# Kernel optimization log

Measured on AMD Instinct MI355X. Metric: run time of the kernel, lower is better.

## Reference

```python
import jax, jax.numpy as jnp
import numpy as np

_CODEBOOK = np.array([
 [-1,-1,-1,-1,-1,-1,-1,-1,-1,-1],[-1,-1,-1,-1,1,1,-1,-1,-1,1],[-1,-1,-1,1,-1,-1,-1,-1,1,1],[-1,-1,-1,1,1,1,-1,-1,1,-1],
 [-1,-1,1,-1,-1,-1,-1,1,1,-1],[-1,-1,1,-1,1,1,-1,1,1,1],[-1,-1,1,1,-1,-1,-1,1,-1,1],[-1,-1,1,1,1,1,-1,1,-1,-1],
 [-1,1,-1,-1,-1,-1,1,1,-1,-1],[-1,1,-1,-1,1,1,1,1,-1,1],[-1,1,-1,1,-1,-1,1,1,1,1],[-1,1,-1,1,1,1,1,1,1,-1],
 [-1,1,1,-1,-1,-1,1,-1,1,-1],[-1,1,1,-1,1,1,1,-1,1,1],[-1,1,1,1,-1,-1,1,-1,-1,1],[-1,1,1,1,1,1,1,-1,-1,-1],
 [1,-1,-1,-1,-1,1,1,-1,-1,-1],[1,-1,-1,-1,1,-1,1,-1,-1,1],[1,-1,-1,1,-1,1,1,-1,1,1],[1,-1,-1,1,1,-1,1,-1,1,-1],
 [1,-1,1,-1,-1,1,1,1,1,-1],[1,-1,1,-1,1,-1,1,1,1,1],[1,-1,1,1,-1,1,1,1,-1,1],[1,-1,1,1,1,-1,1,1,-1,-1],
 [1,1,-1,-1,-1,1,-1,1,-1,-1],[1,1,-1,-1,1,-1,-1,1,-1,1],[1,1,-1,1,-1,1,-1,1,1,1],[1,1,-1,1,1,-1,-1,1,1,-1],
 [1,1,1,-1,-1,1,-1,-1,1,-1],[1,1,1,-1,1,-1,-1,-1,1,1],[1,1,1,1,-1,1,-1,-1,-1,1],[1,1,1,1,1,-1,-1,-1,-1,-1]],
 dtype=np.float32)

def setup_inputs() -> dict:
    key = jax.random.key(0)
    B, N, D = 64, 65536, 10
    signal = jax.random.normal(key, (B, N, D), dtype=jnp.float32)
    codebook = jnp.asarray(_CODEBOOK)  # [32, 10]
    return {"signal": signal, "codebook": codebook}

def reference(signal, codebook):
    # Euclidean distances to all 32 codewords via Gram trick: [B, N, 32]
    x2 = jnp.sum(signal * signal, axis=-1, keepdims=True)          # [B, N, 1]
    c2 = jnp.sum(codebook * codebook, axis=-1)                      # [32]
    xc = jnp.einsum('bnd,kd->bnk', signal, codebook)                # [B, N, 32]
    d2 = jnp.maximum(x2 + c2 - 2.0 * xc, 0.0)
    distances = jnp.sqrt(d2)
    soft_assignments = jax.nn.softmax(-distances, axis=2)           # [B, N, 32]
    most_like = jnp.argmax(soft_assignments, axis=2)                # [B, N]
    softdecision = codebook[most_like]                              # [B, N, 10]
    return softdecision
```

## Files before the change

### kernel.cpp

```cpp
#include <hip/hip_runtime.h>
#include <stdint.h>

#define PTS    256
#define DIM    10
#define STRIDE 11
#define NVEC   ((PTS * DIM) / 4)

__device__ constexpr float CB[32][10] = {
 {-1,-1,-1,-1,-1,-1,-1,-1,-1,-1},{-1,-1,-1,-1,1,1,-1,-1,-1,1},{-1,-1,-1,1,-1,-1,-1,-1,1,1},{-1,-1,-1,1,1,1,-1,-1,1,-1},
 {-1,-1,1,-1,-1,-1,-1,1,1,-1},{-1,-1,1,-1,1,1,-1,1,1,1},{-1,-1,1,1,-1,-1,-1,1,-1,1},{-1,-1,1,1,1,1,-1,1,-1,-1},
 {-1,1,-1,-1,-1,-1,1,1,-1,-1},{-1,1,-1,-1,1,1,1,1,-1,1},{-1,1,-1,1,-1,-1,1,1,1,1},{-1,1,-1,1,1,1,1,1,1,-1},
 {-1,1,1,-1,-1,-1,1,-1,1,-1},{-1,1,1,-1,1,1,1,-1,1,1},{-1,1,1,1,-1,-1,1,-1,-1,1},{-1,1,1,1,1,1,1,-1,-1,-1},
 {1,-1,-1,-1,-1,1,1,-1,-1,-1},{1,-1,-1,-1,1,-1,1,-1,-1,1},{1,-1,-1,1,-1,1,1,-1,1,1},{1,-1,-1,1,1,-1,1,-1,1,-1},
 {1,-1,1,-1,-1,1,1,1,1,-1},{1,-1,1,-1,1,-1,1,1,1,1},{1,-1,1,1,-1,1,1,1,-1,1},{1,-1,1,1,1,-1,1,1,-1,-1},
 {1,1,-1,-1,-1,1,-1,1,-1,-1},{1,1,-1,-1,1,-1,-1,1,-1,1},{1,1,-1,1,-1,1,-1,1,1,1},{1,1,-1,1,1,-1,-1,1,1,-1},
 {1,1,1,-1,-1,1,-1,-1,1,-1},{1,1,1,-1,1,-1,-1,-1,1,1},{1,1,1,1,-1,1,-1,-1,-1,1},{1,1,1,1,1,-1,-1,-1,-1,-1}};

__global__ __launch_bounds__(PTS) void softdec_kernel(
    const float* __restrict__ sig, float* __restrict__ out)
{
    __shared__ float sIn [PTS * STRIDE];
    __shared__ float sOut[PTS * STRIDE];
    const int tid = threadIdx.x;
    const size_t base = (size_t)blockIdx.x * (PTS * DIM);

    const float4* __restrict__ gin = (const float4*)(sig + base);
    #pragma unroll
    for (int it = 0; it < 3; ++it) {
        const int i = tid + it * PTS;
        if (i < NVEC) {
            const float4 v = gin[i];
            const float vv[4] = {v.x, v.y, v.z, v.w};
            #pragma unroll
            for (int j = 0; j < 4; ++j) {
                const int gg = i * 4 + j;
                const int p  = gg / DIM;
                const int c  = gg - p * DIM;
                sIn[p * STRIDE + c] = vv[j];
            }
        }
    }
    __syncthreads();

    float x[DIM];
    #pragma unroll
    for (int j = 0; j < DIM; ++j) x[j] = sIn[tid * STRIDE + j];

    float best = -1e30f;
    int   bi   = 0;
    #pragma unroll
    for (int k = 0; k < 32; ++k) {
        float s = 0.0f;
        #pragma unroll
        for (int j = 0; j < DIM; ++j)
            s = (CB[k][j] > 0.0f) ? (s + x[j]) : (s - x[j]);
        if (s > best) { best = s; bi = k; }
    }

    #pragma unroll
    for (int j = 0; j < DIM; ++j)
        sOut[tid * STRIDE + j] = CB[bi][j];
    __syncthreads();

    float4* __restrict__ gout = (float4*)(out + base);
    #pragma unroll
    for (int it = 0; it < 3; ++it) {
        const int i = tid + it * PTS;
        if (i < NVEC) {
            float4 v;
            float* vv = (float*)&v;
            #pragma unroll
            for (int j = 0; j < 4; ++j) {
                const int gg = i * 4 + j;
                const int p  = gg / DIM;
                const int c  = gg - p * DIM;
                vv[j] = sOut[p * STRIDE + c];
            }
            gout[i] = v;
        }
    }
}

extern "C" void kernel_launch(void* const* d_in, const int* in_sizes, int n_in,
                              void* d_out, int out_size, void* d_ws, size_t ws_size,
                              hipStream_t stream) {
    const float* sig = (const float*)d_in[0];
    float* out = (float*)d_out;
    const int total  = in_sizes[0];
    const int pts    = total / DIM;
    const int blocks = pts / PTS;
    softdec_kernel<<<blocks, PTS, 0, stream>>>(sig, out);
}
```

Baseline: 279.0 us.

## Replace LDS-staged transpose with direct per-thread float2 loads and bitmask output

Drops the shared-memory staging of input and output, along with both barriers and the index divisions. Each thread now reads its own 10 floats as five float2 loads and writes five float2 stores. The output is built from a precomputed per-codeword sign bitmask instead of indexing the codebook table at runtime. The trade-off is less coalesced global access: each thread's accesses are strided 40 bytes apart instead of contiguous float4 accesses across the block.

```diff
diff --git a/kernel.cpp b/kernel.cpp
--- a/kernel.cpp
+++ b/kernel.cpp
@@ -1,12 +1,10 @@
 #include <hip/hip_runtime.h>
 #include <stdint.h>
 
-#define PTS    256
-#define DIM    10
-#define STRIDE 11
-#define NVEC   ((PTS * DIM) / 4)
+#define PTS 256
+#define DIM 10
 
-__device__ constexpr float CB[32][10] = {
+static constexpr float CB[32][10] = {
  {-1,-1,-1,-1,-1,-1,-1,-1,-1,-1},{-1,-1,-1,-1,1,1,-1,-1,-1,1},{-1,-1,-1,1,-1,-1,-1,-1,1,1},{-1,-1,-1,1,1,1,-1,-1,1,-1},
  {-1,-1,1,-1,-1,-1,-1,1,1,-1},{-1,-1,1,-1,1,1,-1,1,1,1},{-1,-1,1,1,-1,-1,-1,1,-1,1},{-1,-1,1,1,1,1,-1,1,-1,-1},
  {-1,1,-1,-1,-1,-1,1,1,-1,-1},{-1,1,-1,-1,1,1,1,1,-1,1},{-1,1,-1,1,-1,-1,1,1,1,1},{-1,1,-1,1,1,1,1,1,1,-1},
@@ -16,68 +14,51 @@
  {1,1,-1,-1,-1,1,-1,1,-1,-1},{1,1,-1,-1,1,-1,-1,1,-1,1},{1,1,-1,1,-1,1,-1,1,1,1},{1,1,-1,1,1,-1,-1,1,1,-1},
  {1,1,1,-1,-1,1,-1,-1,1,-1},{1,1,1,-1,1,-1,-1,-1,1,1},{1,1,1,1,-1,1,-1,-1,-1,1},{1,1,1,1,1,-1,-1,-1,-1,-1}};
 
+struct CBMasks { uint32_t m[32]; };
+static constexpr CBMasks make_masks() {
+    CBMasks r{};
+    for (int k = 0; k < 32; ++k) {
+        uint32_t mm = 0;
+        for (int j = 0; j < DIM; ++j)
+            if (CB[k][j] > 0.0f) mm |= (1u << j);
+        r.m[k] = mm;
+    }
+    return r;
+}
+static constexpr CBMasks CBM = make_masks();
+
 __global__ __launch_bounds__(PTS) void softdec_kernel(
     const float* __restrict__ sig, float* __restrict__ out)
 {
-    __shared__ float sIn [PTS * STRIDE];
-    __shared__ float sOut[PTS * STRIDE];
-    const int tid = threadIdx.x;
-    const size_t base = (size_t)blockIdx.x * (PTS * DIM);
+    const size_t p = (size_t)blockIdx.x * PTS + threadIdx.x;
 
-    const float4* __restrict__ gin = (const float4*)(sig + base);
-    #pragma unroll
-    for (int it = 0; it < 3; ++it) {
-        const int i = tid + it * PTS;
-        if (i < NVEC) {
-            const float4 v = gin[i];
-            const float vv[4] = {v.x, v.y, v.z, v.w};
-            #pragma unroll
-            for (int j = 0; j < 4; ++j) {
-                const int gg = i * 4 + j;
-                const int p  = gg / DIM;
-                const int c  = gg - p * DIM;
-                sIn[p * STRIDE + c] = vv[j];
-            }
-        }
-    }
-    __syncthreads();
-
+    const float2* __restrict__ gp = (const float2*)sig + p * 5;
     float x[DIM];
     #pragma unroll
-    for (int j = 0; j < DIM; ++j) x[j] = sIn[tid * STRIDE + j];
+    for (int q = 0; q < 5; ++q) {
+        const float2 v = gp[q];
+        x[2 * q]     = v.x;
+        x[2 * q + 1] = v.y;
+    }
 
-    float best = -1e30f;
-    int   bi   = 0;
+    float    best = -1e30f;
+    uint32_t bm   = 0u;
     #pragma unroll
     for (int k = 0; k < 32; ++k) {
         float s = 0.0f;
         #pragma unroll
         for (int j = 0; j < DIM; ++j)
             s = (CB[k][j] > 0.0f) ? (s + x[j]) : (s - x[j]);
-        if (s > best) { best = s; bi = k; }
+        if (s > best) { best = s; bm = CBM.m[k]; }
     }
 
+    float2* __restrict__ op = (float2*)out + p * 5;
     #pragma unroll
-    for (int j = 0; j < DIM; ++j)
-        sOut[tid * STRIDE + j] = CB[bi][j];
-    __syncthreads();
-
-    float4* __restrict__ gout = (float4*)(out + base);
-    #pragma unroll
-    for (int it = 0; it < 3; ++it) {
-        const int i = tid + it * PTS;
-        if (i < NVEC) {
-            float4 v;
-            float* vv = (float*)&v;
-            #pragma unroll
-            for (int j = 0; j < 4; ++j) {
-                const int gg = i * 4 + j;
-                const int p  = gg / DIM;
-                const int c  = gg - p * DIM;
-                vv[j] = sOut[p * STRIDE + c];
-            }
-            gout[i] = v;
-        }
+    for (int q = 0; q < 5; ++q) {
+        float2 v;
+        v.x = __uint_as_float(0xBF800000u ^ (((bm >> (2 * q))     & 1u) << 31));
+        v.y = __uint_as_float(0xBF800000u ^ (((bm >> (2 * q + 1)) & 1u) << 31));
+        op[q] = v;
     }
 }
 
```

New measurement: 281.8 us. No clear change (+1.0%).
